# Performance work log

Hardware: AMD Instinct MI355X
Metric: run time of the kernel (lower is better)

Reference implementation:

```python
import jax, jax.numpy as jnp
import numpy as np

B, S, D = 4, 4096, 256

def setup_inputs() -> dict:
    key = jax.random.key(0)
    ks = jax.random.split(key, 7)
    s = 1.0 / np.sqrt(D)
    return {
        "x": jax.random.normal(ks[0], (B, S, D), dtype=jnp.float32),
        "Wq": jax.random.normal(ks[1], (D, D), dtype=jnp.float32) * s,
        "bq": jax.random.normal(ks[2], (D,), dtype=jnp.float32) * s,
        "Wk": jax.random.normal(ks[3], (D, D), dtype=jnp.float32) * s,
        "bk": jax.random.normal(ks[4], (D,), dtype=jnp.float32) * s,
        "Wv": jax.random.normal(ks[5], (D, D), dtype=jnp.float32) * s,
        "bv": jax.random.normal(ks[6], (D,), dtype=jnp.float32) * s,
    }

def reference(x, Wq, bq, Wk, bk, Wv, bv):
    # nn.Linear: y = x @ W.T + b
    q = jnp.einsum('bsd,ed->bse', x, Wq) + bq  # [B,S,D]
    k = jnp.einsum('bsd,ed->bse', x, Wk) + bk  # [B,S,D]
    v = jnp.einsum('bsd,ed->bse', x, Wv) + bv  # [B,S,D]
    scale = 1.0 / jnp.sqrt(jnp.float32(x.shape[-1]))
    scores = jnp.einsum('bqd,bkd->bqk', q, k) * scale  # [B,S,S]
    attn = jax.nn.softmax(scores, axis=-1)
    return jnp.einsum('bqk,bkd->bqd', attn, v)
```

## Files before the change

### kernel.cpp

```cpp
#include <hip/hip_runtime.h>

typedef __attribute__((ext_vector_type(8))) short bf16x8;
typedef __attribute__((ext_vector_type(4))) short bf16x4;
typedef __attribute__((ext_vector_type(4))) float f32x4;
typedef __attribute__((ext_vector_type(16))) float f32x16;

#define MFMA16(a,b,c) __builtin_amdgcn_mfma_f32_16x16x32_bf16((a),(b),(c),0,0,0)
#define MFMA32(a,b,c) __builtin_amdgcn_mfma_f32_32x32x16_bf16((a),(b),(c),0,0,0)

__device__ __forceinline__ short f2bf(float f) {
  union { float f; unsigned u; } v; v.f = f;
  unsigned r = v.u + 0x7FFFu + ((v.u >> 16) & 1u);
  return (short)(r >> 16);
}
__device__ __forceinline__ float bf2f(short s) {
  union { unsigned u; float f; } v; v.u = ((unsigned)(unsigned short)s) << 16;
  return v.f;
}
__device__ __forceinline__ unsigned cvtpk(float lo, float hi) {
  unsigned d;
  asm("v_cvt_pk_bf16_f32 %0, %1, %2" : "=v"(d) : "v"(lo), "v"(hi));
  return d;
}
__device__ __forceinline__ void async16(const void* g, void* l) {
  __builtin_amdgcn_global_load_lds(
      (const __attribute__((address_space(1))) unsigned*)g,
      (__attribute__((address_space(3))) unsigned*)l, 16, 0, 0);
}

__global__ void cvt_w_kernel(const float* __restrict__ Wq, const float* __restrict__ Wk,
                             const float* __restrict__ Wv, short* __restrict__ Wb) {
  int v = blockIdx.x * 256 + threadIdx.x;
  int z = v >> 13, r = v & 8191;
  const float* src = ((z == 0) ? Wq : (z == 1) ? Wk : Wv) + r * 8;
  float4 a = *(const float4*)src;
  float4 b = *(const float4*)(src + 4);
  bf16x8 h;
  h[0]=f2bf(a.x); h[1]=f2bf(a.y); h[2]=f2bf(a.z); h[3]=f2bf(a.w);
  h[4]=f2bf(b.x); h[5]=f2bf(b.y); h[6]=f2bf(b.z); h[7]=f2bf(b.w);
  *(bf16x8*)(Wb + z * 65536 + r * 8) = h;
}

__global__ __launch_bounds__(256, 2) void proj_kernel(
    const float* __restrict__ x, const short* __restrict__ Wb,
    const float* __restrict__ bq, const float* __restrict__ bk, const float* __restrict__ bv,
    short* __restrict__ Qb, short* __restrict__ Kb, short* __restrict__ VTb)
{
  __shared__ __attribute__((aligned(16))) char xs[32768];
  const int tid = threadIdx.x;
  const int lane = tid & 63;
  const int w = tid >> 6;
  const int l15 = lane & 15, lg = lane >> 4;
  const int z = blockIdx.x >> 8;
  const int mtile = blockIdx.x & 255;
  const int m0 = mtile * 64;
  const int batch = m0 >> 12;
  const int s0 = m0 & 4095;

  #pragma unroll
  for (int c = 0; c < 8; ++c) {
    int v = c * 256 + tid;
    int row = v >> 5, u = v & 31;
    const float* g = x + (size_t)(m0 + row) * 256 + u * 8;
    float4 a = *(const float4*)g;
    float4 b = *(const float4*)(g + 4);
    bf16x8 h;
    h[0]=f2bf(a.x); h[1]=f2bf(a.y); h[2]=f2bf(a.z); h[3]=f2bf(a.w);
    h[4]=f2bf(b.x); h[5]=f2bf(b.y); h[6]=f2bf(b.z); h[7]=f2bf(b.w);
    *(bf16x8*)(xs + row * 512 + ((u ^ (row & 31)) * 16)) = h;
  }
  __syncthreads();

  const short* Wz = Wb + z * 65536;
  bf16x8 wf[4][8];
  #pragma unroll
  for (int fc = 0; fc < 4; ++fc)
    #pragma unroll
    for (int ks = 0; ks < 8; ++ks)
      wf[fc][ks] = *(const bf16x8*)(Wz + (size_t)(w*64 + fc*16 + l15) * 256 + ks*32 + lg*8);

  if (z < 2) {
    const float* bias = z ? bk : bq;
    short* Ob = z ? Kb : Qb;
    const float scl = z ? 1.0f : 0.0625f;
    float bb[4][4];
    #pragma unroll
    for (int fc = 0; fc < 4; ++fc)
      #pragma unroll
      for (int r = 0; r < 4; ++r) bb[fc][r] = bias[w*64 + fc*16 + lg*4 + r];
    #pragma unroll
    for (int ms = 0; ms < 4; ++ms) {
      bf16x8 xa[8];
      #pragma unroll
      for (int ks = 0; ks < 8; ++ks) {
        int row = ms * 16 + l15;
        xa[ks] = *(const bf16x8*)(xs + row * 512 + (((ks*4 + lg) ^ (row & 31)) * 16));
      }
      f32x4 acc[4];
      #pragma unroll
      for (int fc = 0; fc < 4; ++fc) acc[fc] = (f32x4){0.f,0.f,0.f,0.f};
      #pragma unroll
      for (int ks = 0; ks < 8; ++ks)
        #pragma unroll
        for (int fc = 0; fc < 4; ++fc)
          acc[fc] = MFMA16(wf[fc][ks], xa[ks], acc[fc]);
      #pragma unroll
      for (int fc = 0; fc < 4; ++fc) {
        bf16x4 pv;
        #pragma unroll
        for (int r = 0; r < 4; ++r) pv[r] = f2bf((acc[fc][r] + bb[fc][r]) * scl);
        *(bf16x4*)(Ob + (size_t)(m0 + ms*16 + l15) * 256 + w*64 + fc*16 + lg*4) = pv;
      }
    }
  } else {
    float bvr[4];
    #pragma unroll
    for (int fc = 0; fc < 4; ++fc) bvr[fc] = bv[w*64 + fc*16 + l15];
    #pragma unroll
    for (int ms = 0; ms < 4; ++ms) {
      bf16x8 xa[8];
      #pragma unroll
      for (int ks = 0; ks < 8; ++ks) {
        int row = ms * 16 + l15;
        xa[ks] = *(const bf16x8*)(xs + row * 512 + (((ks*4 + lg) ^ (row & 31)) * 16));
      }
      f32x4 acc[4];
      #pragma unroll
      for (int fc = 0; fc < 4; ++fc) acc[fc] = (f32x4){0.f,0.f,0.f,0.f};
      #pragma unroll
      for (int ks = 0; ks < 8; ++ks)
        #pragma unroll
        for (int fc = 0; fc < 4; ++fc)
          acc[fc] = MFMA16(xa[ks], wf[fc][ks], acc[fc]);
      #pragma unroll
      for (int fc = 0; fc < 4; ++fc) {
        bf16x4 pv;
        #pragma unroll
        for (int r = 0; r < 4; ++r) pv[r] = f2bf(acc[fc][r] + bvr[fc]);
        *(bf16x4*)(VTb + (size_t)(batch*256 + w*64 + fc*16 + l15) * 4096 + s0 + ms*16 + lg*4) = pv;
      }
    }
  }
}

__global__ __launch_bounds__(512, 2) void attn_kernel(
    const short* __restrict__ Qb, const short* __restrict__ Kb,
    const short* __restrict__ VTb, short* __restrict__ Op, float* __restrict__ mlg)
{
  __shared__ __attribute__((aligned(16))) char smem[131072];
  const int tid = threadIdx.x;
  const int lane = tid & 63;
  const int w = tid >> 6;
  const int l31 = lane & 31, hi = lane >> 5;

  const int b = blockIdx.x;
  const int c = b & 15;
  const int batch = c >> 2, ns = c & 3;
  const int qt = b >> 4;
  const int q0 = qt * 256;
  const int kvbase = ns * 1024;

  const char* Kg = (const char*)(Kb  + (size_t)batch * 4096 * 256);
  const char* Vg = (const char*)(VTb + (size_t)batch * 256 * 4096);

  bf16x8 qf[16];
  {
    const short* qrow = Qb + (size_t)(batch*4096 + q0 + w*32 + l31) * 256;
    #pragma unroll
    for (int ks = 0; ks < 16; ++ks) qf[ks] = *(const bf16x8*)(qrow + ks*16 + hi*8);
  }

  f32x16 o[8];
  #pragma unroll
  for (int i = 0; i < 8; ++i)
    #pragma unroll
    for (int r = 0; r < 16; ++r) o[i][r] = 0.f;
  float m_run = -1e30f, l_run = 0.f;

  auto stage = [&](int buf, int kv0) {
    char* kl = smem + buf * 32768;
    #pragma unroll
    for (int cc = 0; cc < 2; ++cc) {
      int v = cc * 512 + tid;
      int row = v >> 5, s = v & 31;
      async16(Kg + (size_t)(kvbase ? 0 : 0) + (size_t)(kv0 + row) * 512 + ((s ^ row) * 16),
              kl + (size_t)v * 16);
    }
    char* vl = smem + buf * 32768 + 16384;
    #pragma unroll
    for (int cc = 0; cc < 2; ++cc) {
      int v = cc * 512 + tid;
      int sr = v >> 5, j = v & 31;
      int jun = j ^ sr;
      int d = sr * 8 + (jun >> 2), u = jun & 3;
      async16(Vg + (size_t)d * 8192 + (size_t)kv0 * 2 + u * 16,
              vl + (size_t)v * 16);
    }
  };

  stage(0, kvbase);
  stage(1, kvbase + 32);
  stage(2, kvbase + 64);

  for (int t = 0; t < 32; ++t) {
    if (t < 30)       asm volatile("s_waitcnt vmcnt(8)" ::: "memory");
    else if (t == 30) asm volatile("s_waitcnt vmcnt(4)" ::: "memory");
    else              asm volatile("s_waitcnt vmcnt(0)" ::: "memory");
    __builtin_amdgcn_sched_barrier(0);
    __builtin_amdgcn_s_barrier();
    __builtin_amdgcn_sched_barrier(0);
    if (t < 29) stage((t + 3) & 3, kvbase + (t + 3) * 32);

    const char* kl = smem + (t & 3) * 32768;
    const char* vl = kl + 16384;

    f32x16 st;
    #pragma unroll
    for (int r = 0; r < 16; ++r) st[r] = 0.f;
    __builtin_amdgcn_s_setprio(1);
    #pragma unroll
    for (int ks = 0; ks < 16; ++ks) {
      bf16x8 kf = *(const bf16x8*)(kl + l31 * 512 + (((ks*2 + hi) ^ l31) * 16));
      st = MFMA32(kf, qf[ks], st);
    }
    __builtin_amdgcn_s_setprio(0);

    float mx = st[0];
    #pragma unroll
    for (int r = 1; r < 16; ++r) mx = fmaxf(mx, st[r]);
    mx = fmaxf(mx, __shfl_xor(mx, 32));
    float m_new = fmaxf(m_run, mx);
    if (m_new > m_run) {
      float alpha = __expf(m_run - m_new);
      l_run *= alpha;
      #pragma unroll
      for (int df = 0; df < 8; ++df) o[df] = o[df] * alpha;
      m_run = m_new;
    }
    float lsum = 0.f;
    #pragma unroll
    for (int r = 0; r < 16; ++r) { st[r] = __expf(st[r] - m_run); lsum += st[r]; }
    l_run += lsum;

    bf16x8 pa[2];
    #pragma unroll
    for (int kvf = 0; kvf < 2; ++kvf) {
      unsigned X  = cvtpk(st[8*kvf+0], st[8*kvf+1]);
      unsigned X2 = cvtpk(st[8*kvf+2], st[8*kvf+3]);
      unsigned Y  = cvtpk(st[8*kvf+4], st[8*kvf+5]);
      unsigned Y2 = cvtpk(st[8*kvf+6], st[8*kvf+7]);
      unsigned Xs  = __shfl_xor((int)X, 32);
      unsigned X2s = __shfl_xor((int)X2, 32);
      unsigned Ys  = __shfl_xor((int)Y, 32);
      unsigned Y2s = __shfl_xor((int)Y2, 32);
      union { unsigned u[4]; bf16x8 v; } fr;
      fr.u[0] = hi ? Ys  : X;
      fr.u[1] = hi ? Y2s : X2;
      fr.u[2] = hi ? Y   : Xs;
      fr.u[3] = hi ? Y2  : X2s;
      pa[kvf] = fr.v;
    }

    __builtin_amdgcn_s_setprio(1);
    #pragma unroll
    for (int kvf = 0; kvf < 2; ++kvf) {
      #pragma unroll
      for (int df = 0; df < 8; ++df) {
        int sr = df * 4 + (l31 >> 3);
        int j = ((l31 & 7) * 4 + kvf * 2 + hi) ^ sr;
        bf16x8 vb = *(const bf16x8*)(vl + sr * 512 + j * 16);
        o[df] = MFMA32(vb, pa[kvf], o[df]);
      }
    }
    __builtin_amdgcn_s_setprio(0);
  }

  float lt = l_run + __shfl_xor(l_run, 32);
  const int qglob = batch*4096 + q0 + w*32 + l31;
  short* op = Op + ((size_t)ns * 16384 + qglob) * 256;
  #pragma unroll
  for (int df = 0; df < 8; ++df)
    #pragma unroll
    for (int g = 0; g < 4; ++g) {
      bf16x4 pv;
      #pragma unroll
      for (int cc = 0; cc < 4; ++cc) pv[cc] = f2bf(o[df][4*g + cc]);
      *(bf16x4*)(op + df*32 + 8*g + 4*hi) = pv;
    }
  if (!hi) {
    mlg[((size_t)ns*16384 + qglob)*2]     = m_run;
    mlg[((size_t)ns*16384 + qglob)*2 + 1] = lt;
  }
}

__global__ void combine_kernel(const short* __restrict__ Op, const float* __restrict__ mlg,
                               float* __restrict__ out) {
  int idx = blockIdx.x * 256 + threadIdx.x;
  int row = idx >> 5, c = idx & 31;
  float m[4], l[4];
  #pragma unroll
  for (int p = 0; p < 4; ++p) {
    m[p] = mlg[((size_t)p*16384 + row)*2];
    l[p] = mlg[((size_t)p*16384 + row)*2 + 1];
  }
  float ms = fmaxf(fmaxf(m[0], m[1]), fmaxf(m[2], m[3]));
  float a[4], den = 0.f;
  #pragma unroll
  for (int p = 0; p < 4; ++p) { a[p] = __expf(m[p] - ms); den += a[p]*l[p]; }
  float inv = 1.0f / den;
  float acc[8];
  #pragma unroll
  for (int j = 0; j < 8; ++j) acc[j] = 0.f;
  #pragma unroll
  for (int p = 0; p < 4; ++p) {
    bf16x8 v = *(const bf16x8*)(Op + ((size_t)p*16384 + row)*256 + c*8);
    #pragma unroll
    for (int j = 0; j < 8; ++j) acc[j] += a[p] * bf2f(v[j]);
  }
  float4 r0 = {acc[0]*inv, acc[1]*inv, acc[2]*inv, acc[3]*inv};
  float4 r1 = {acc[4]*inv, acc[5]*inv, acc[6]*inv, acc[7]*inv};
  float* po = out + (size_t)row * 256 + c * 8;
  *(float4*)po = r0;
  *(float4*)(po + 4) = r1;
}

extern "C" void kernel_launch(void* const* d_in, const int* in_sizes, int n_in,
                              void* d_out, int out_size, void* d_ws, size_t ws_size,
                              hipStream_t stream) {
  const float* x  = (const float*)d_in[0];
  const float* Wq = (const float*)d_in[1];
  const float* bq = (const float*)d_in[2];
  const float* Wk = (const float*)d_in[3];
  const float* bk = (const float*)d_in[4];
  const float* Wv = (const float*)d_in[5];
  const float* bv = (const float*)d_in[6];
  float* out = (float*)d_out;

  char* ws = (char*)d_ws;
  short* Qb  = (short*)(ws);
  short* Kb  = (short*)(ws + 8388608);
  short* VTb = (short*)(ws + 16777216);
  short* Wb  = (short*)(ws + 25165824);
  float* mlg = (float*)(ws + 25559040);
  short* Op  = (short*)(ws + 26083328);

  cvt_w_kernel<<<dim3(96), dim3(256), 0, stream>>>(Wq, Wk, Wv, Wb);
  proj_kernel<<<dim3(768), dim3(256), 0, stream>>>(x, Wb, bq, bk, bv, Qb, Kb, VTb);
  attn_kernel<<<dim3(256), dim3(512), 0, stream>>>(Qb, Kb, VTb, Op, mlg);
  combine_kernel<<<dim3(2048), dim3(256), 0, stream>>>(Op, mlg, out);
}
```

Before: 225.5 us.

## Pre-convert x to bf16, async-load in projection, shrink attention blocks to 4 waves

Adds a separate kernel that converts x to bf16 once, so each of the three projection passes loads it into LDS with async global-to-LDS copies and no longer re-converts fp32 per z. The attention kernel moves from 8 waves with 256 query rows and a 4-deep LDS ring to 4 waves with 128 query rows and 64KB double buffering, launching twice as many blocks. The aim is more blocks per CU and less wasted conversion work, at the cost of an extra launch, a shallower prefetch pipeline and an extra barrier per iteration. xb reuses the Op workspace region, which is safe only because proj finishes before attn writes Op.

```diff
diff --git a/kernel.cpp b/kernel.cpp
--- a/kernel.cpp
+++ b/kernel.cpp
@@ -41,8 +41,19 @@
   *(bf16x8*)(Wb + z * 65536 + r * 8) = h;
 }
 
+__global__ void cvt_x_kernel(const float* __restrict__ x, short* __restrict__ xb) {
+  int v = blockIdx.x * 256 + threadIdx.x;
+  const float* src = x + (size_t)v * 8;
+  float4 a = *(const float4*)src;
+  float4 b = *(const float4*)(src + 4);
+  bf16x8 h;
+  h[0]=f2bf(a.x); h[1]=f2bf(a.y); h[2]=f2bf(a.z); h[3]=f2bf(a.w);
+  h[4]=f2bf(b.x); h[5]=f2bf(b.y); h[6]=f2bf(b.z); h[7]=f2bf(b.w);
+  *(bf16x8*)(xb + (size_t)v * 8) = h;
+}
+
 __global__ __launch_bounds__(256, 2) void proj_kernel(
-    const float* __restrict__ x, const short* __restrict__ Wb,
+    const short* __restrict__ xb, const short* __restrict__ Wb,
     const float* __restrict__ bq, const float* __restrict__ bk, const float* __restrict__ bv,
     short* __restrict__ Qb, short* __restrict__ Kb, short* __restrict__ VTb)
 {
@@ -57,19 +68,13 @@
   const int batch = m0 >> 12;
   const int s0 = m0 & 4095;
 
+  const char* xg = (const char*)(xb) + (size_t)m0 * 512;
   #pragma unroll
   for (int c = 0; c < 8; ++c) {
     int v = c * 256 + tid;
     int row = v >> 5, u = v & 31;
-    const float* g = x + (size_t)(m0 + row) * 256 + u * 8;
-    float4 a = *(const float4*)g;
-    float4 b = *(const float4*)(g + 4);
-    bf16x8 h;
-    h[0]=f2bf(a.x); h[1]=f2bf(a.y); h[2]=f2bf(a.z); h[3]=f2bf(a.w);
-    h[4]=f2bf(b.x); h[5]=f2bf(b.y); h[6]=f2bf(b.z); h[7]=f2bf(b.w);
-    *(bf16x8*)(xs + row * 512 + ((u ^ (row & 31)) * 16)) = h;
-  }
-  __syncthreads();
+    async16(xg + (size_t)row * 512 + ((u ^ (row & 31)) * 16), xs + (size_t)v * 16);
+  }
 
   const short* Wz = Wb + z * 65536;
   bf16x8 wf[4][8];
@@ -78,6 +83,8 @@
     #pragma unroll
     for (int ks = 0; ks < 8; ++ks)
       wf[fc][ks] = *(const bf16x8*)(Wz + (size_t)(w*64 + fc*16 + l15) * 256 + ks*32 + lg*8);
+
+  __syncthreads();
 
   if (z < 2) {
     const float* bias = z ? bk : bq;
@@ -143,11 +150,11 @@
   }
 }
 
-__global__ __launch_bounds__(512, 2) void attn_kernel(
+__global__ __launch_bounds__(256, 2) void attn_kernel(
     const short* __restrict__ Qb, const short* __restrict__ Kb,
     const short* __restrict__ VTb, short* __restrict__ Op, float* __restrict__ mlg)
 {
-  __shared__ __attribute__((aligned(16))) char smem[131072];
+  __shared__ __attribute__((aligned(16))) char smem[65536];
   const int tid = threadIdx.x;
   const int lane = tid & 63;
   const int w = tid >> 6;
@@ -157,7 +164,7 @@
   const int c = b & 15;
   const int batch = c >> 2, ns = c & 3;
   const int qt = b >> 4;
-  const int q0 = qt * 256;
+  const int q0 = qt * 128;
   const int kvbase = ns * 1024;
 
   const char* Kg = (const char*)(Kb  + (size_t)batch * 4096 * 256);
@@ -180,38 +187,37 @@
   auto stage = [&](int buf, int kv0) {
     char* kl = smem + buf * 32768;
     #pragma unroll
-    for (int cc = 0; cc < 2; ++cc) {
-      int v = cc * 512 + tid;
+    for (int cc = 0; cc < 4; ++cc) {
+      int v = cc * 256 + tid;
       int row = v >> 5, s = v & 31;
-      async16(Kg + (size_t)(kvbase ? 0 : 0) + (size_t)(kv0 + row) * 512 + ((s ^ row) * 16),
-              kl + (size_t)v * 16);
+      async16(Kg + (size_t)(kv0 + row) * 512 + ((s ^ row) * 16), kl + (size_t)v * 16);
     }
     char* vl = smem + buf * 32768 + 16384;
     #pragma unroll
-    for (int cc = 0; cc < 2; ++cc) {
-      int v = cc * 512 + tid;
+    for (int cc = 0; cc < 4; ++cc) {
+      int v = cc * 256 + tid;
       int sr = v >> 5, j = v & 31;
       int jun = j ^ sr;
       int d = sr * 8 + (jun >> 2), u = jun & 3;
-      async16(Vg + (size_t)d * 8192 + (size_t)kv0 * 2 + u * 16,
-              vl + (size_t)v * 16);
+      async16(Vg + (size_t)d * 8192 + (size_t)kv0 * 2 + u * 16, vl + (size_t)v * 16);
     }
   };
 
   stage(0, kvbase);
-  stage(1, kvbase + 32);
-  stage(2, kvbase + 64);
 
   for (int t = 0; t < 32; ++t) {
-    if (t < 30)       asm volatile("s_waitcnt vmcnt(8)" ::: "memory");
-    else if (t == 30) asm volatile("s_waitcnt vmcnt(4)" ::: "memory");
-    else              asm volatile("s_waitcnt vmcnt(0)" ::: "memory");
+    const int cur = t & 1;
+    if (t < 31) {
+      stage(cur ^ 1, kvbase + (t + 1) * 32);
+      asm volatile("s_waitcnt vmcnt(8)" ::: "memory");
+    } else {
+      asm volatile("s_waitcnt vmcnt(0)" ::: "memory");
+    }
     __builtin_amdgcn_sched_barrier(0);
     __builtin_amdgcn_s_barrier();
     __builtin_amdgcn_sched_barrier(0);
-    if (t < 29) stage((t + 3) & 3, kvbase + (t + 3) * 32);
-
-    const char* kl = smem + (t & 3) * 32768;
+
+    const char* kl = smem + cur * 32768;
     const char* vl = kl + 16384;
 
     f32x16 st;
@@ -273,6 +279,9 @@
       }
     }
     __builtin_amdgcn_s_setprio(0);
+
+    __builtin_amdgcn_sched_barrier(0);
+    __builtin_amdgcn_s_barrier();
   }
 
   float lt = l_run + __shfl_xor(l_run, 32);
@@ -343,9 +352,11 @@
   short* Wb  = (short*)(ws + 25165824);
   float* mlg = (float*)(ws + 25559040);
   short* Op  = (short*)(ws + 26083328);
+  short* xb  = (short*)(ws + 26083328);
 
   cvt_w_kernel<<<dim3(96), dim3(256), 0, stream>>>(Wq, Wk, Wv, Wb);
-  proj_kernel<<<dim3(768), dim3(256), 0, stream>>>(x, Wb, bq, bk, bv, Qb, Kb, VTb);
-  attn_kernel<<<dim3(256), dim3(512), 0, stream>>>(Qb, Kb, VTb, Op, mlg);
+  cvt_x_kernel<<<dim3(2048), dim3(256), 0, stream>>>(x, xb);
+  proj_kernel<<<dim3(768), dim3(256), 0, stream>>>(xb, Wb, bq, bk, bv, Qb, Kb, VTb);
+  attn_kernel<<<dim3(512), dim3(256), 0, stream>>>(Qb, Kb, VTb, Op, mlg);
   combine_kernel<<<dim3(2048), dim3(256), 0, stream>>>(Op, mlg, out);
 }
```

Measured after the change: 262.1 us. +16.2%, slower.
